# Optimization experiments

Measured on AMD Instinct MI355X. Metric: run time of the kernel, lower is better.

## Reference

```python
import math
import jax, jax.numpy as jnp
import numpy as np

B, S, E, H = 4, 2048, 1024, 16
HD = E // H  # 64


def setup_inputs() -> dict:
    key = jax.random.key(0)
    ks = jax.random.split(key, 7)
    scale = 1.0 / math.sqrt(E)
    return {
        "x": jax.random.normal(ks[0], (B, S, E), dtype=jnp.float32),
        "Wq": jax.random.normal(ks[1], (H, HD, E), dtype=jnp.float32) * scale,
        "bq": jax.random.normal(ks[2], (H, HD), dtype=jnp.float32) * 0.01,
        "Wk": jax.random.normal(ks[3], (H, HD, E), dtype=jnp.float32) * scale,
        "bk": jax.random.normal(ks[4], (H, HD), dtype=jnp.float32) * 0.01,
        "Wv": jax.random.normal(ks[5], (H, HD, E), dtype=jnp.float32) * scale,
        "bv": jax.random.normal(ks[6], (H, HD), dtype=jnp.float32) * 0.01,
    }


def reference(x, Wq, bq, Wk, bk, Wv, bv):
    b, s, e = x.shape
    h, hd, _ = Wq.shape
    inv_scale = 1.0 / math.sqrt(hd)
    # per-head linear projections (torch Linear: x @ W^T + b), batched over heads
    q = jnp.einsum("bse,hde->bshd", x, Wq) + bq  # [B,S,H,HD]
    k = jnp.einsum("bse,hde->bshd", x, Wk) + bk
    v = jnp.einsum("bse,hde->bshd", x, Wv) + bv
    # causal mask: -inf above diagonal (added before scaling, as in source;
    # -inf * inv_scale is still -inf so math is identical)
    mask = jnp.triu(jnp.full((s, s), -jnp.inf, dtype=x.dtype), k=1)
    scores = (jnp.einsum("bqhd,bkhd->bhqk", q, k) + mask) * inv_scale  # [B,H,S,S]
    attn = jax.nn.softmax(scores, axis=-1)
    out = jnp.einsum("bhqk,bkhd->bqhd", attn, v)  # [B,S,H,HD]
    # concat over heads in head order == reshape with head-major last dims
    return out.reshape(b, s, h * hd)
```

## Files before the change

kernel.cpp:

```cpp
#include <hip/hip_runtime.h>


typedef __bf16 bf16x8 __attribute__((ext_vector_type(8)));
typedef __bf16 bf16x4 __attribute__((ext_vector_type(4)));
typedef float f32x4 __attribute__((ext_vector_type(4)));
typedef unsigned short us8 __attribute__((ext_vector_type(8)));
typedef unsigned short us4 __attribute__((ext_vector_type(4)));

#define Bb 4
#define Ss 2048
#define Ee 1024
#define Hh 16
#define HD 64

#if __has_builtin(__builtin_amdgcn_exp2f)
#define EXP2(x) __builtin_amdgcn_exp2f(x)
#else
#define EXP2(x) exp2f(x)
#endif

__device__ __forceinline__ unsigned short f2bf(float f) {
  union { float f; unsigned u; } v; v.f = f;
  unsigned u = v.u;
  u += 0x7fffu + ((u >> 16) & 1u);
  return (unsigned short)(u >> 16);
}

__device__ __forceinline__ void gl_lds16(const void* g, void* l) {
  __builtin_amdgcn_global_load_lds((const __attribute__((address_space(1))) void*)g,
                                   (__attribute__((address_space(3))) void*)l, 16, 0, 0);
}

__global__ __launch_bounds__(256) void cvt_all(const float* __restrict__ x,
                                               const float* __restrict__ wq,
                                               const float* __restrict__ wk,
                                               const float* __restrict__ wv,
                                               unsigned short* __restrict__ xb,
                                               unsigned short* __restrict__ wb) {
  int i = blockIdx.x * 256 + threadIdx.x;
  const float* src; unsigned short* dst; int idx;
  if (i < 2097152)      { src = x;  dst = xb;                idx = i; }
  else if (i < 2359296) { src = wq; dst = wb;                idx = i - 2097152; }
  else if (i < 2621440) { src = wk; dst = wb + 1048576;      idx = i - 2359296; }
  else                  { src = wv; dst = wb + 2 * 1048576;  idx = i - 2621440; }
  float4 f = ((const float4*)src)[idx];
  us4 o = { f2bf(f.x), f2bf(f.y), f2bf(f.z), f2bf(f.w) };
  ((us4*)dst)[idx] = o;
}

__global__ __launch_bounds__(256) void qkv_gemm(const unsigned short* __restrict__ xb,
                                                const unsigned short* __restrict__ wb_all,
                                                const float* __restrict__ bq,
                                                const float* __restrict__ bk,
                                                const float* __restrict__ bv,
                                                unsigned short* __restrict__ qkv) {
  const int z = blockIdx.z;
  const unsigned short* wb = wb_all + (size_t)z * (Ee * Ee);
  const float* bias = (z == 0) ? bq : (z == 1) ? bk : bv;
  unsigned short* outb = qkv + (size_t)z * (Bb * Ss * Ee);
  const float osc = (z == 0) ? 0.180336880f : 1.0f;

  __shared__ unsigned short SMEM[16384];
  unsigned short* As = SMEM;
  unsigned short* Bs = SMEM + 8192;

  const int t = threadIdx.x;
  const int wave = t >> 6, lane = t & 63, quad = lane >> 4, ln = lane & 15;
  const int wm = wave & 1, wn = wave >> 1;
  const int m0 = blockIdx.x * 128, n0 = blockIdx.y * 128;

  const int srow = t >> 2;
  const int scol = (t & 3) * 8;

  f32x4 acc[4][4] = {};

  const unsigned short* ga = xb + (size_t)(m0 + srow) * Ee + scol;
  const unsigned short* gb = wb + (size_t)(n0 + srow) * Ee + scol;
  unsigned short* la = &As[t * 8];
  unsigned short* lb = &Bs[t * 8];

  for (int k0 = 0; k0 < Ee; k0 += 64) {
    __syncthreads();
    gl_lds16(ga + k0,                la);
    gl_lds16(ga + k0 + 64 * Ee,      la + 64 * 32);
    gl_lds16(gb + k0,                lb);
    gl_lds16(gb + k0 + 64 * Ee,      lb + 64 * 32);
    gl_lds16(ga + k0 + 32,           la + 4096);
    gl_lds16(ga + k0 + 32 + 64 * Ee, la + 4096 + 64 * 32);
    gl_lds16(gb + k0 + 32,           lb + 4096);
    gl_lds16(gb + k0 + 32 + 64 * Ee, lb + 4096 + 64 * 32);
    __syncthreads();
#pragma unroll
    for (int p = 0; p < 2; ++p) {
      bf16x8 af[4], bfr[4];
#pragma unroll
      for (int i = 0; i < 4; ++i)
        af[i] = *(const bf16x8*)&As[p * 4096 + (wm * 64 + i * 16 + ln) * 32 + quad * 8];
#pragma unroll
      for (int j = 0; j < 4; ++j)
        bfr[j] = *(const bf16x8*)&Bs[p * 4096 + (wn * 64 + j * 16 + ln) * 32 + quad * 8];
#pragma unroll
      for (int i = 0; i < 4; ++i)
#pragma unroll
        for (int j = 0; j < 4; ++j)
          acc[i][j] = __builtin_amdgcn_mfma_f32_16x16x32_bf16(af[i], bfr[j], acc[i][j], 0, 0, 0);
    }
  }

  float biasj[4];
#pragma unroll
  for (int j = 0; j < 4; ++j) biasj[j] = bias[n0 + wn * 64 + j * 16 + ln];

  if (z != 2) {
#pragma unroll
    for (int i = 0; i < 4; ++i)
#pragma unroll
      for (int j = 0; j < 4; ++j)
#pragma unroll
        for (int r = 0; r < 4; ++r) {
          int m = m0 + wm * 64 + i * 16 + quad * 4 + r;
          int n = n0 + wn * 64 + j * 16 + ln;
          int b_ = m >> 11, s = m & 2047;
          int h = n >> 6, d = n & 63;
          outb[(((size_t)b_ * Hh + h) * Ss + s) * HD + d] = f2bf((acc[i][j][r] + biasj[j]) * osc);
        }
  } else {
    for (int half = 0; half < 2; ++half) {
      __syncthreads();
      if (wm == half) {
#pragma unroll
        for (int i = 0; i < 4; ++i)
#pragma unroll
          for (int j = 0; j < 4; ++j)
#pragma unroll
            for (int r = 0; r < 4; ++r) {
              int mr = i * 16 + quad * 4 + r;
              int nc = wn * 64 + j * 16 + ln;
              SMEM[nc * 72 + mr] = f2bf(acc[i][j][r] + biasj[j]);
            }
      }
      __syncthreads();
      int nr = t >> 1;
      int n = n0 + nr;
      int h = n >> 6, d = n & 63;
      int mbase = m0 + half * 64 + (t & 1) * 32;
      int b_ = mbase >> 11;
#pragma unroll
      for (int q = 0; q < 4; ++q) {
        int s = (mbase & 2047) + q * 8;
        us8 vdat = *(const us8*)&SMEM[nr * 72 + (t & 1) * 32 + q * 8];
        *(us8*)&outb[(((size_t)b_ * Hh + h) * HD + d) * Ss + s] = vdat;
      }
    }
  }
}

__global__ __launch_bounds__(256) void flash_attn(const unsigned short* __restrict__ qkv,
                                                  float* __restrict__ out) {
  const int id = blockIdx.x;
  const int bh = id & 63;
  const int pair = id >> 6;
  const int b_ = bh >> 4, h = bh & 15;

  const unsigned short* qb  = qkv + (size_t)bh * (Ss * HD);
  const unsigned short* kb  = qkv + (size_t)(64 + bh) * (Ss * HD);
  const unsigned short* vtb = qkv + (size_t)(128 + bh) * (Ss * HD);

  __shared__ __bf16 Ks[4096];
  __shared__ __bf16 Vt[4096];
  __shared__ __bf16 Ps[4][16][72];

  const int t = threadIdx.x;
  const int wave = t >> 6, lane = t & 63, quad = lane >> 4, ln = lane & 15;

  const int r0 = t >> 3;
  const int c0 = ((t & 7) ^ (r0 & 7)) * 8;
  const int koff0 = r0 * HD + c0;
  const int koff1 = koff0 + 32 * HD;
  const int voff0 = r0 * Ss + c0;
  const int voff1 = voff0 + 32 * Ss;
  __bf16* Kl0 = &Ks[t * 8];  __bf16* Kl1 = &Ks[2048 + t * 8];
  __bf16* Vl0 = &Vt[t * 8];  __bf16* Vl1 = &Vt[2048 + t * 8];

  int kslot[4][2];
#pragma unroll
  for (int g = 0; g < 4; ++g)
#pragma unroll
    for (int ks = 0; ks < 2; ++ks)
      kslot[g][ks] = ((g * 16 + ln) * 8 + ((ks * 4 + quad) ^ (ln & 7))) * 8;

  bf16x8 onef;
#pragma unroll
  for (int j = 0; j < 8; ++j) onef[j] = (__bf16)1.0f;

  const int qts[2] = { 31 - pair, pair };

  for (int ph = 0; ph < 2; ++ph) {
    const int qt = qts[ph];
    const int q0 = qt * 64;
    const int qrow = q0 + wave * 16 + ln;

    bf16x8 qf[2];
#pragma unroll
    for (int ks = 0; ks < 2; ++ks)
      qf[ks] = *(const bf16x8*)(qb + (size_t)qrow * HD + ks * 32 + quad * 8);

    f32x4 o[4] = {};
    f32x4 l4 = {};

    for (int kt = 0; kt <= qt; ++kt) {
      const unsigned short* kbt = kb + kt * (64 * HD);
      const unsigned short* vbt = vtb + kt * 64;
      __syncthreads();
      gl_lds16(kbt + koff0, Kl0);
      gl_lds16(kbt + koff1, Kl1);
      gl_lds16(vbt + voff0, Vl0);
      gl_lds16(vbt + voff1, Vl1);
      __syncthreads();

      f32x4 s_acc[4] = {};
#pragma unroll
      for (int g = 0; g < 4; ++g)
#pragma unroll
        for (int ks = 0; ks < 2; ++ks) {
          bf16x8 kf = *(const bf16x8*)&Ks[kslot[g][ks]];
          s_acc[g] = __builtin_amdgcn_mfma_f32_16x16x32_bf16(kf, qf[ks], s_acc[g], 0, 0, 0);
        }

      if (kt == qt) {
        const int k0 = kt * 64;
#pragma unroll
        for (int g = 0; g < 4; ++g)
#pragma unroll
          for (int r = 0; r < 4; ++r) {
            int kcol = k0 + g * 16 + quad * 4 + r;
            if (kcol > qrow) s_acc[g][r] = -__builtin_inff();
          }
      }

#pragma unroll
      for (int g = 0; g < 4; ++g) {
        bf16x4 pk = { (__bf16)EXP2(s_acc[g][0]), (__bf16)EXP2(s_acc[g][1]),
                      (__bf16)EXP2(s_acc[g][2]), (__bf16)EXP2(s_acc[g][3]) };
        *(bf16x4*)&Ps[wave][ln][g * 16 + quad * 4] = pk;
      }
      bf16x8 pf[2];
#pragma unroll
      for (int ks = 0; ks < 2; ++ks)
        pf[ks] = *(const bf16x8*)&Ps[wave][ln][ks * 32 + quad * 8];

      l4 = __builtin_amdgcn_mfma_f32_16x16x32_bf16(pf[0], onef, l4, 0, 0, 0);
      l4 = __builtin_amdgcn_mfma_f32_16x16x32_bf16(pf[1], onef, l4, 0, 0, 0);

#pragma unroll
      for (int g = 0; g < 4; ++g)
#pragma unroll
        for (int ks = 0; ks < 2; ++ks) {
          bf16x8 vf = *(const bf16x8*)&Vt[kslot[g][ks]];
          o[g] = __builtin_amdgcn_mfma_f32_16x16x32_bf16(pf[ks], vf, o[g], 0, 0, 0);
        }
    }

    float linv[4];
#pragma unroll
    for (int r = 0; r < 4; ++r) linv[r] = 1.0f / l4[r];
#pragma unroll
    for (int g = 0; g < 4; ++g)
#pragma unroll
      for (int r = 0; r < 4; ++r) {
        int orow = q0 + wave * 16 + quad * 4 + r;
        out[((size_t)b_ * Ss + orow) * Ee + h * HD + g * 16 + ln] = o[g][r] * linv[r];
      }
    __syncthreads();
  }
}

extern "C" void kernel_launch(void* const* d_in, const int* in_sizes, int n_in,
                              void* d_out, int out_size, void* d_ws, size_t ws_size,
                              hipStream_t stream) {
  const float* x  = (const float*)d_in[0];
  const float* Wq = (const float*)d_in[1];
  const float* bq = (const float*)d_in[2];
  const float* Wk = (const float*)d_in[3];
  const float* bk = (const float*)d_in[4];
  const float* Wv = (const float*)d_in[5];
  const float* bv = (const float*)d_in[6];
  float* out = (float*)d_out;

  unsigned short* ws  = (unsigned short*)d_ws;
  unsigned short* xb  = ws;
  unsigned short* wb  = ws + 8388608;
  unsigned short* qkv = ws + 8388608 + 3 * 1048576;

  cvt_all<<<11264, 256, 0, stream>>>(x, Wq, Wk, Wv, xb, wb);
  qkv_gemm<<<dim3(64, 8, 3), 256, 0, stream>>>(xb, wb, bq, bk, bv, qkv);
  flash_attn<<<1024, 256, 0, stream>>>(qkv, out);
}
```

Before: 219.5 us.

## Process two query tiles per block to reuse each K/V tile load

```diff
diff --git a/kernel.cpp b/kernel.cpp
--- a/kernel.cpp
+++ b/kernel.cpp
@@ -159,7 +159,7 @@
                                                   float* __restrict__ out) {
   const int id = blockIdx.x;
   const int bh = id & 63;
-  const int pair = id >> 6;
+  const int p = id >> 6;
   const int b_ = bh >> 4, h = bh & 15;
 
   const unsigned short* qb  = qkv + (size_t)bh * (Ss * HD);
@@ -168,7 +168,7 @@
 
   __shared__ __bf16 Ks[4096];
   __shared__ __bf16 Vt[4096];
-  __shared__ __bf16 Ps[4][16][72];
+  __shared__ __bf16 Ps[4][2][16][72];
 
   const int t = threadIdx.x;
   const int wave = t >> 6, lane = t & 63, quad = lane >> 4, ln = lane & 15;
@@ -193,22 +193,25 @@
 #pragma unroll
   for (int j = 0; j < 8; ++j) onef[j] = (__bf16)1.0f;
 
-  const int qts[2] = { 31 - pair, pair };
+  const int qtps[2] = { 15 - p, p };
 
   for (int ph = 0; ph < 2; ++ph) {
-    const int qt = qts[ph];
-    const int q0 = qt * 64;
-    const int qrow = q0 + wave * 16 + ln;
-
-    bf16x8 qf[2];
-#pragma unroll
-    for (int ks = 0; ks < 2; ++ks)
-      qf[ks] = *(const bf16x8*)(qb + (size_t)qrow * HD + ks * 32 + quad * 8);
-
-    f32x4 o[4] = {};
-    f32x4 l4 = {};
-
-    for (int kt = 0; kt <= qt; ++kt) {
+    const int qtp = qtps[ph];
+    const int q0 = qtp * 128;
+
+    bf16x8 qf[2][2];
+#pragma unroll
+    for (int u = 0; u < 2; ++u)
+#pragma unroll
+      for (int ks = 0; ks < 2; ++ks)
+        qf[u][ks] = *(const bf16x8*)(qb + (size_t)(q0 + u * 64 + wave * 16 + ln) * HD +
+                                     ks * 32 + quad * 8);
+
+    f32x4 o[2][4] = {};
+    f32x4 l4[2] = {};
+    const int ktmax = 2 * qtp + 1;
+
+    for (int kt = 0; kt <= ktmax; ++kt) {
       const unsigned short* kbt = kb + kt * (64 * HD);
       const unsigned short* vbt = vtb + kt * 64;
       __syncthreads();
@@ -218,59 +221,68 @@
       gl_lds16(vbt + voff1, Vl1);
       __syncthreads();
 
-      f32x4 s_acc[4] = {};
-#pragma unroll
-      for (int g = 0; g < 4; ++g)
-#pragma unroll
-        for (int ks = 0; ks < 2; ++ks) {
-          bf16x8 kf = *(const bf16x8*)&Ks[kslot[g][ks]];
-          s_acc[g] = __builtin_amdgcn_mfma_f32_16x16x32_bf16(kf, qf[ks], s_acc[g], 0, 0, 0);
+#pragma unroll
+      for (int u = 0; u < 2; ++u) {
+        if (u == 0 && kt == ktmax) continue;
+        const int qrow = q0 + u * 64 + wave * 16 + ln;
+
+        f32x4 s_acc[4] = {};
+#pragma unroll
+        for (int g = 0; g < 4; ++g)
+#pragma unroll
+          for (int ks = 0; ks < 2; ++ks) {
+            bf16x8 kf = *(const bf16x8*)&Ks[kslot[g][ks]];
+            s_acc[g] = __builtin_amdgcn_mfma_f32_16x16x32_bf16(kf, qf[u][ks], s_acc[g], 0, 0, 0);
+          }
+
+        if (kt == 2 * qtp + u) {
+          const int k0 = kt * 64;
+#pragma unroll
+          for (int g = 0; g < 4; ++g)
+#pragma unroll
+            for (int r = 0; r < 4; ++r) {
+              int kcol = k0 + g * 16 + quad * 4 + r;
+              if (kcol > qrow) s_acc[g][r] = -__builtin_inff();
+            }
         }
 
-      if (kt == qt) {
-        const int k0 = kt * 64;
+#pragma unroll
+        for (int g = 0; g < 4; ++g) {
+          bf16x4 pk = { (__bf16)EXP2(s_acc[g][0]), (__bf16)EXP2(s_acc[g][1]),
+                        (__bf16)EXP2(s_acc[g][2]), (__bf16)EXP2(s_acc[g][3]) };
+          *(bf16x4*)&Ps[wave][u][ln][g * 16 + quad * 4] = pk;
+        }
+        bf16x8 pf[2];
+#pragma unroll
+        for (int ks = 0; ks < 2; ++ks)
+          pf[ks] = *(const bf16x8*)&Ps[wave][u][ln][ks * 32 + quad * 8];
+
+        l4[u] = __builtin_amdgcn_mfma_f32_16x16x32_bf16(pf[0], onef, l4[u], 0, 0, 0);
+        l4[u] = __builtin_amdgcn_mfma_f32_16x16x32_bf16(pf[1], onef, l4[u], 0, 0, 0);
+
 #pragma unroll
         for (int g = 0; g < 4; ++g)
 #pragma unroll
-          for (int r = 0; r < 4; ++r) {
-            int kcol = k0 + g * 16 + quad * 4 + r;
-            if (kcol > qrow) s_acc[g][r] = -__builtin_inff();
+          for (int ks = 0; ks < 2; ++ks) {
+            bf16x8 vf = *(const bf16x8*)&Vt[kslot[g][ks]];
+            o[u][g] = __builtin_amdgcn_mfma_f32_16x16x32_bf16(pf[ks], vf, o[u][g], 0, 0, 0);
           }
       }
-
-#pragma unroll
-      for (int g = 0; g < 4; ++g) {
-        bf16x4 pk = { (__bf16)EXP2(s_acc[g][0]), (__bf16)EXP2(s_acc[g][1]),
-                      (__bf16)EXP2(s_acc[g][2]), (__bf16)EXP2(s_acc[g][3]) };
-        *(bf16x4*)&Ps[wave][ln][g * 16 + quad * 4] = pk;
-      }
-      bf16x8 pf[2];
-#pragma unroll
-      for (int ks = 0; ks < 2; ++ks)
-        pf[ks] = *(const bf16x8*)&Ps[wave][ln][ks * 32 + quad * 8];
-
-      l4 = __builtin_amdgcn_mfma_f32_16x16x32_bf16(pf[0], onef, l4, 0, 0, 0);
-      l4 = __builtin_amdgcn_mfma_f32_16x16x32_bf16(pf[1], onef, l4, 0, 0, 0);
-
+    }
+
+#pragma unroll
+    for (int u = 0; u < 2; ++u) {
+      float linv[4];
+#pragma unroll
+      for (int r = 0; r < 4; ++r) linv[r] = 1.0f / l4[u][r];
 #pragma unroll
       for (int g = 0; g < 4; ++g)
 #pragma unroll
-        for (int ks = 0; ks < 2; ++ks) {
-          bf16x8 vf = *(const bf16x8*)&Vt[kslot[g][ks]];
-          o[g] = __builtin_amdgcn_mfma_f32_16x16x32_bf16(pf[ks], vf, o[g], 0, 0, 0);
+        for (int r = 0; r < 4; ++r) {
+          int orow = q0 + u * 64 + wave * 16 + quad * 4 + r;
+          out[((size_t)b_ * Ss + orow) * Ee + h * HD + g * 16 + ln] = o[u][g][r] * linv[r];
         }
     }
-
-    float linv[4];
-#pragma unroll
-    for (int r = 0; r < 4; ++r) linv[r] = 1.0f / l4[r];
-#pragma unroll
-    for (int g = 0; g < 4; ++g)
-#pragma unroll
-      for (int r = 0; r < 4; ++r) {
-        int orow = q0 + wave * 16 + quad * 4 + r;
-        out[((size_t)b_ * Ss + orow) * Ee + h * HD + g * 16 + ln] = o[g][r] * linv[r];
-      }
     __syncthreads();
   }
 }
@@ -294,5 +306,5 @@
 
   cvt_all<<<11264, 256, 0, stream>>>(x, Wq, Wk, Wv, xb, wb);
   qkv_gemm<<<dim3(64, 8, 3), 256, 0, stream>>>(xb, wb, bq, bk, bv, qkv);
-  flash_attn<<<1024, 256, 0, stream>>>(qkv, out);
-}
+  flash_attn<<<512, 256, 0, stream>>>(qkv, out);
+}
```

After: 218.1 us. Within noise of the previous version (-0.6%).

## Split KV tiles across waves in flash attention with LDS reduction of partial outputs

Applied to the files above, without the earlier changes.

```diff
diff --git a/kernel.cpp b/kernel.cpp
--- a/kernel.cpp
+++ b/kernel.cpp
@@ -48,12 +48,12 @@
   ((us4*)dst)[idx] = o;
 }
 
-__global__ __launch_bounds__(256) void qkv_gemm(const unsigned short* __restrict__ xb,
-                                                const unsigned short* __restrict__ wb_all,
-                                                const float* __restrict__ bq,
-                                                const float* __restrict__ bk,
-                                                const float* __restrict__ bv,
-                                                unsigned short* __restrict__ qkv) {
+__global__ __launch_bounds__(256, 3) void qkv_gemm(const unsigned short* __restrict__ xb,
+                                                   const unsigned short* __restrict__ wb_all,
+                                                   const float* __restrict__ bq,
+                                                   const float* __restrict__ bk,
+                                                   const float* __restrict__ bv,
+                                                   unsigned short* __restrict__ qkv) {
   const int z = blockIdx.z;
   const unsigned short* wb = wb_all + (size_t)z * (Ee * Ee);
   const float* bias = (z == 0) ? bq : (z == 1) ? bk : bv;
@@ -155,122 +155,154 @@
   }
 }
 
-__global__ __launch_bounds__(256) void flash_attn(const unsigned short* __restrict__ qkv,
-                                                  float* __restrict__ out) {
+__global__ __launch_bounds__(256, 2) void flash_attn(const unsigned short* __restrict__ qkv,
+                                                     float* __restrict__ out) {
   const int id = blockIdx.x;
   const int bh = id & 63;
-  const int pair = id >> 6;
+  const int p = id >> 6;
   const int b_ = bh >> 4, h = bh & 15;
 
   const unsigned short* qb  = qkv + (size_t)bh * (Ss * HD);
   const unsigned short* kb  = qkv + (size_t)(64 + bh) * (Ss * HD);
   const unsigned short* vtb = qkv + (size_t)(128 + bh) * (Ss * HD);
 
-  __shared__ __bf16 Ks[4096];
-  __shared__ __bf16 Vt[4096];
-  __shared__ __bf16 Ps[4][16][72];
+  __shared__ char SM[36864];
+  __bf16* Ps   = (__bf16*)SM;
+  float*  bufA = (float*)SM;
+  float*  bufB = (float*)(SM + 17408);
+  __shared__ float Lbuf[4][64];
 
   const int t = threadIdx.x;
   const int wave = t >> 6, lane = t & 63, quad = lane >> 4, ln = lane & 15;
-
-  const int r0 = t >> 3;
-  const int c0 = ((t & 7) ^ (r0 & 7)) * 8;
-  const int koff0 = r0 * HD + c0;
-  const int koff1 = koff0 + 32 * HD;
-  const int voff0 = r0 * Ss + c0;
-  const int voff1 = voff0 + 32 * Ss;
-  __bf16* Kl0 = &Ks[t * 8];  __bf16* Kl1 = &Ks[2048 + t * 8];
-  __bf16* Vl0 = &Vt[t * 8];  __bf16* Vl1 = &Vt[2048 + t * 8];
-
-  int kslot[4][2];
-#pragma unroll
-  for (int g = 0; g < 4; ++g)
-#pragma unroll
-    for (int ks = 0; ks < 2; ++ks)
-      kslot[g][ks] = ((g * 16 + ln) * 8 + ((ks * 4 + quad) ^ (ln & 7))) * 8;
+  __bf16* Pw = Ps + wave * (64 * 72);
 
   bf16x8 onef;
 #pragma unroll
   for (int j = 0; j < 8; ++j) onef[j] = (__bf16)1.0f;
 
-  const int qts[2] = { 31 - pair, pair };
+  const int qts[2] = { 31 - p, p };
 
   for (int ph = 0; ph < 2; ++ph) {
     const int qt = qts[ph];
     const int q0 = qt * 64;
-    const int qrow = q0 + wave * 16 + ln;
-
-    bf16x8 qf[2];
-#pragma unroll
-    for (int ks = 0; ks < 2; ++ks)
-      qf[ks] = *(const bf16x8*)(qb + (size_t)qrow * HD + ks * 32 + quad * 8);
-
-    f32x4 o[4] = {};
-    f32x4 l4 = {};
-
-    for (int kt = 0; kt <= qt; ++kt) {
-      const unsigned short* kbt = kb + kt * (64 * HD);
-      const unsigned short* vbt = vtb + kt * 64;
-      __syncthreads();
-      gl_lds16(kbt + koff0, Kl0);
-      gl_lds16(kbt + koff1, Kl1);
-      gl_lds16(vbt + voff0, Vl0);
-      gl_lds16(vbt + voff1, Vl1);
-      __syncthreads();
-
-      f32x4 s_acc[4] = {};
-#pragma unroll
-      for (int g = 0; g < 4; ++g)
-#pragma unroll
-        for (int ks = 0; ks < 2; ++ks) {
-          bf16x8 kf = *(const bf16x8*)&Ks[kslot[g][ks]];
-          s_acc[g] = __builtin_amdgcn_mfma_f32_16x16x32_bf16(kf, qf[ks], s_acc[g], 0, 0, 0);
+
+    bf16x8 qf[4][2];
+#pragma unroll
+    for (int gb = 0; gb < 4; ++gb)
+#pragma unroll
+      for (int ks = 0; ks < 2; ++ks)
+        qf[gb][ks] = *(const bf16x8*)(qb + (size_t)(q0 + gb * 16 + ln) * HD + ks * 32 + quad * 8);
+
+    f32x4 o[4][4] = {};
+    f32x4 l4[4]  = {};
+
+    for (int kt = wave; kt <= qt; kt += 4) {
+      const unsigned short* kbase = kb + (size_t)kt * (64 * HD);
+      bf16x8 kf[4][2], vf[4][2];
+#pragma unroll
+      for (int ga = 0; ga < 4; ++ga)
+#pragma unroll
+        for (int ks = 0; ks < 2; ++ks)
+          kf[ga][ks] = *(const bf16x8*)(kbase + (size_t)(ga * 16 + ln) * HD + ks * 32 + quad * 8);
+#pragma unroll
+      for (int gd = 0; gd < 4; ++gd)
+#pragma unroll
+        for (int ks = 0; ks < 2; ++ks)
+          vf[gd][ks] = *(const bf16x8*)(vtb + (size_t)(gd * 16 + ln) * Ss + kt * 64 + ks * 32 + quad * 8);
+      const bool diag = (kt == qt);
+
+#pragma unroll
+      for (int gb = 0; gb < 4; ++gb) {
+        f32x4 s[4] = {};
+#pragma unroll
+        for (int ga = 0; ga < 4; ++ga)
+#pragma unroll
+          for (int ks = 0; ks < 2; ++ks)
+            s[ga] = __builtin_amdgcn_mfma_f32_16x16x32_bf16(kf[ga][ks], qf[gb][ks], s[ga], 0, 0, 0);
+
+#pragma unroll
+        for (int ga = 0; ga < 4; ++ga) {
+          float pv[4];
+#pragma unroll
+          for (int r = 0; r < 4; ++r) {
+            float e = EXP2(s[ga][r]);
+            pv[r] = (diag && (ga * 16 + quad * 4 + r > gb * 16 + ln)) ? 0.f : e;
+          }
+          bf16x4 pk = { (__bf16)pv[0], (__bf16)pv[1], (__bf16)pv[2], (__bf16)pv[3] };
+          *(bf16x4*)&Pw[(gb * 16 + ln) * 72 + ga * 16 + quad * 4] = pk;
         }
-
-      if (kt == qt) {
-        const int k0 = kt * 64;
-#pragma unroll
-        for (int g = 0; g < 4; ++g)
-#pragma unroll
-          for (int r = 0; r < 4; ++r) {
-            int kcol = k0 + g * 16 + quad * 4 + r;
-            if (kcol > qrow) s_acc[g][r] = -__builtin_inff();
-          }
+        bf16x8 pf0 = *(const bf16x8*)&Pw[(gb * 16 + ln) * 72 + quad * 8];
+        bf16x8 pf1 = *(const bf16x8*)&Pw[(gb * 16 + ln) * 72 + 32 + quad * 8];
+
+        l4[gb] = __builtin_amdgcn_mfma_f32_16x16x32_bf16(onef, pf0, l4[gb], 0, 0, 0);
+        l4[gb] = __builtin_amdgcn_mfma_f32_16x16x32_bf16(onef, pf1, l4[gb], 0, 0, 0);
+
+#pragma unroll
+        for (int gd = 0; gd < 4; ++gd) {
+          o[gd][gb] = __builtin_amdgcn_mfma_f32_16x16x32_bf16(vf[gd][0], pf0, o[gd][gb], 0, 0, 0);
+          o[gd][gb] = __builtin_amdgcn_mfma_f32_16x16x32_bf16(vf[gd][1], pf1, o[gd][gb], 0, 0, 0);
+        }
       }
-
-#pragma unroll
-      for (int g = 0; g < 4; ++g) {
-        bf16x4 pk = { (__bf16)EXP2(s_acc[g][0]), (__bf16)EXP2(s_acc[g][1]),
-                      (__bf16)EXP2(s_acc[g][2]), (__bf16)EXP2(s_acc[g][3]) };
-        *(bf16x4*)&Ps[wave][ln][g * 16 + quad * 4] = pk;
+    }
+
+    if (quad == 0) {
+#pragma unroll
+      for (int gb = 0; gb < 4; ++gb) Lbuf[wave][gb * 16 + ln] = l4[gb][0];
+    }
+    __syncthreads();
+    if (wave == 0) {
+#pragma unroll
+      for (int gd = 0; gd < 4; ++gd)
+#pragma unroll
+        for (int gb = 0; gb < 4; ++gb)
+#pragma unroll
+          for (int r = 0; r < 4; ++r)
+            bufA[(gd * 16 + quad * 4 + r) * 68 + gb * 16 + ln] = o[gd][gb][r];
+    } else if (wave == 1) {
+#pragma unroll
+      for (int gd = 0; gd < 4; ++gd)
+#pragma unroll
+        for (int gb = 0; gb < 4; ++gb)
+#pragma unroll
+          for (int r = 0; r < 4; ++r)
+            bufB[(gd * 16 + quad * 4 + r) * 68 + gb * 16 + ln] = o[gd][gb][r];
+    }
+    __syncthreads();
+    if (wave == 2) {
+#pragma unroll
+      for (int gd = 0; gd < 4; ++gd)
+#pragma unroll
+        for (int gb = 0; gb < 4; ++gb)
+#pragma unroll
+          for (int r = 0; r < 4; ++r)
+            bufA[(gd * 16 + quad * 4 + r) * 68 + gb * 16 + ln] += o[gd][gb][r];
+    } else if (wave == 3) {
+#pragma unroll
+      for (int gd = 0; gd < 4; ++gd)
+#pragma unroll
+        for (int gb = 0; gb < 4; ++gb)
+#pragma unroll
+          for (int r = 0; r < 4; ++r)
+            bufB[(gd * 16 + quad * 4 + r) * 68 + gb * 16 + ln] += o[gd][gb][r];
+    }
+    __syncthreads();
+    {
+      const int q = t >> 2;
+      const int dbase = (t & 3) * 16;
+      float ltot = Lbuf[0][q] + Lbuf[1][q] + Lbuf[2][q] + Lbuf[3][q];
+      float linv = 1.0f / ltot;
+      float* op = out + ((size_t)b_ * Ss + q0 + q) * Ee + h * HD + dbase;
+#pragma unroll
+      for (int c = 0; c < 4; ++c) {
+        int d = dbase + c * 4;
+        float4 vv;
+        vv.x = (bufA[(d + 0) * 68 + q] + bufB[(d + 0) * 68 + q]) * linv;
+        vv.y = (bufA[(d + 1) * 68 + q] + bufB[(d + 1) * 68 + q]) * linv;
+        vv.z = (bufA[(d + 2) * 68 + q] + bufB[(d + 2) * 68 + q]) * linv;
+        vv.w = (bufA[(d + 3) * 68 + q] + bufB[(d + 3) * 68 + q]) * linv;
+        ((float4*)op)[c] = vv;
       }
-      bf16x8 pf[2];
-#pragma unroll
-      for (int ks = 0; ks < 2; ++ks)
-        pf[ks] = *(const bf16x8*)&Ps[wave][ln][ks * 32 + quad * 8];
-
-      l4 = __builtin_amdgcn_mfma_f32_16x16x32_bf16(pf[0], onef, l4, 0, 0, 0);
-      l4 = __builtin_amdgcn_mfma_f32_16x16x32_bf16(pf[1], onef, l4, 0, 0, 0);
-
-#pragma unroll
-      for (int g = 0; g < 4; ++g)
-#pragma unroll
-        for (int ks = 0; ks < 2; ++ks) {
-          bf16x8 vf = *(const bf16x8*)&Vt[kslot[g][ks]];
-          o[g] = __builtin_amdgcn_mfma_f32_16x16x32_bf16(pf[ks], vf, o[g], 0, 0, 0);
-        }
-    }
-
-    float linv[4];
-#pragma unroll
-    for (int r = 0; r < 4; ++r) linv[r] = 1.0f / l4[r];
-#pragma unroll
-    for (int g = 0; g < 4; ++g)
-#pragma unroll
-      for (int r = 0; r < 4; ++r) {
-        int orow = q0 + wave * 16 + quad * 4 + r;
-        out[((size_t)b_ * Ss + orow) * Ee + h * HD + g * 16 + ln] = o[g][r] * linv[r];
-      }
+    }
     __syncthreads();
   }
 }
```

New measurement: 232.5 us. +5.9%, slower.
